# Kernel optimization log

Hardware: AMD Instinct MI355X
Metric: run time of the kernel (lower is better)

The kernel has to match this reference:

```python
import jax, jax.numpy as jnp
import numpy as np

H = 64  # hidden_size


def gru_layer(x, h0, W_ih, W_hh, b_ih, b_hh):
    """PyTorch-convention GRU layer. x: [B,T,D], h0: [B,H]. Returns ([B,T,H], [B,H])."""
    # Precompute input-side gate projections with one big GEMM: [B,T,3H]
    gx_all = jnp.einsum('btd,gd->btg', x, W_ih) + b_ih

    def step(h, gx):
        gh = h @ W_hh.T + b_hh                      # [B,3H]
        xr, xz, xn = jnp.split(gx, 3, axis=-1)
        hr, hz, hn = jnp.split(gh, 3, axis=-1)
        r = jax.nn.sigmoid(xr + hr)
        z = jax.nn.sigmoid(xz + hz)
        n = jnp.tanh(xn + r * hn)
        h_new = (1.0 - z) * n + z * h
        return h_new, h_new

    hT, hs = jax.lax.scan(step, h0, jnp.swapaxes(gx_all, 0, 1))  # hs: [T,B,H]
    return jnp.swapaxes(hs, 0, 1), hT


def setup_inputs() -> dict:
    key = jax.random.key(0)
    ks = jax.random.split(key, 16)
    B, T, D = 256, 2048, 1
    x = jax.random.normal(ks[0], (B, T, D), dtype=jnp.float32)
    h0 = jnp.zeros((2, B, H), dtype=jnp.float32)
    s = 1.0 / np.sqrt(H)
    # Layer 0: input_size=1
    W_ih0 = jax.random.normal(ks[1], (3 * H, D), dtype=jnp.float32) * s
    W_hh0 = jax.random.normal(ks[2], (3 * H, H), dtype=jnp.float32) * s
    b_ih0 = jnp.zeros((3 * H,), dtype=jnp.float32)
    b_hh0 = jnp.zeros((3 * H,), dtype=jnp.float32)
    # Layer 1: input_size=H
    W_ih1 = jax.random.normal(ks[3], (3 * H, H), dtype=jnp.float32) * s
    W_hh1 = jax.random.normal(ks[4], (3 * H, H), dtype=jnp.float32) * s
    b_ih1 = jnp.zeros((3 * H,), dtype=jnp.float32)
    b_hh1 = jnp.zeros((3 * H,), dtype=jnp.float32)
    # Head: Linear(H,H) -> ReLU -> Linear(H,1)
    Wh1 = jax.random.normal(ks[5], (H, H), dtype=jnp.float32) * s
    bh1 = jnp.zeros((H,), dtype=jnp.float32)
    Wh2 = jax.random.normal(ks[6], (1, H), dtype=jnp.float32) * s
    bh2 = jnp.zeros((1,), dtype=jnp.float32)
    return {"x": x, "h0": h0, "W_ih0": W_ih0, "W_hh0": W_hh0, "b_ih0": b_ih0,
            "b_hh0": b_hh0, "W_ih1": W_ih1, "W_hh1": W_hh1, "b_ih1": b_ih1,
            "b_hh1": b_hh1, "Wh1": Wh1, "bh1": bh1, "Wh2": Wh2, "bh2": bh2}


def reference(x, h0, W_ih0, W_hh0, b_ih0, b_hh0, W_ih1, W_hh1, b_ih1, b_hh1,
              Wh1, bh1, Wh2, bh2):
    z0, hT0 = gru_layer(x, h0[0], W_ih0, W_hh0, b_ih0, b_hh0)
    z1, hT1 = gru_layer(z0, h0[1], W_ih1, W_hh1, b_ih1, b_hh1)
    hT = jnp.stack([hT0, hT1], axis=0)           # [2,B,H]
    h = jax.nn.relu(jnp.einsum('bth,oh->bto', z1, Wh1) + bh1)
    y = jnp.einsum('bth,oh->bto', h, Wh2) + bh2  # [B,T,1]
    return (y, hT)
```

## Files before the change

### kernel.cpp

```cpp
#include <hip/hip_runtime.h>

#define HH 64
#define TT 2048
#define BB 256
#define YSZ (BB*TT)

__device__ __forceinline__ float sigmoid_f(float v) {
    return 1.0f / (1.0f + __expf(-v));
}
__device__ __forceinline__ float tanh_f(float v) {
    return 1.0f - 2.0f / (1.0f + __expf(2.0f * v));
}

__global__ __launch_bounds__(512, 2)
void gru_fused(const float* __restrict__ x,
               const float* __restrict__ h0in,
               const float* __restrict__ W_ih0,
               const float* __restrict__ W_hh0,
               const float* __restrict__ b_ih0,
               const float* __restrict__ b_hh0,
               const float* __restrict__ W_ih1,
               const float* __restrict__ W_hh1,
               const float* __restrict__ b_ih1,
               const float* __restrict__ b_hh1,
               const float* __restrict__ Wh1,
               const float* __restrict__ bh1,
               const float* __restrict__ Wh2,
               const float* __restrict__ bh2,
               float* __restrict__ out)
{
    const int b    = blockIdx.x;
    const int tid  = threadIdx.x;
    const int t    = tid & 255;
    const int half = tid >> 8;
    const int ko   = half << 5;

    __shared__ __align__(16) float h0_lds[HH];
    __shared__ __align__(16) float h1_lds[HH];
    __shared__ __align__(16) float part[2 * 192 * 4];
    __shared__ __align__(16) float ph[2 * 64];
    __shared__ __align__(16) float x_lds[TT];

    {
        const float4* xs = reinterpret_cast<const float4*>(x + (size_t)b * TT);
        float4*       xd = reinterpret_cast<float4*>(x_lds);
        for (int k = tid; k < TT / 4; k += 512) xd[k] = xs[k];
    }
    if (tid < HH) {
        h0_lds[tid] = h0in[           b * HH + tid];
        h1_lds[tid] = h0in[BB * HH +  b * HH + tid];
    }

    float4 wA[8], wB[8], wC[8];
    float bA = 0.f, bB = 0.f, bC = 0.f;
    if (t < 192) {
        const float4* pa = reinterpret_cast<const float4*>(W_hh0 + t * HH + ko);
        const float4* pb = reinterpret_cast<const float4*>(W_ih1 + t * HH + ko);
        const float4* pc = reinterpret_cast<const float4*>(W_hh1 + t * HH + ko);
        #pragma unroll
        for (int k = 0; k < 8; ++k) { wA[k] = pa[k]; wB[k] = pb[k]; wC[k] = pc[k]; }
        if (half == 0) { bA = b_hh0[t]; bB = b_ih1[t]; bC = b_hh1[t]; }
    } else {
        const float4* pa = reinterpret_cast<const float4*>(Wh1 + (t - 192) * HH + ko);
        #pragma unroll
        for (int k = 0; k < 8; ++k) { wA[k] = pa[k]; wB[k] = pa[k]; wC[k] = pa[k]; }
    }
    float wih0_r = 0.f, wih0_z = 0.f, wih0_n = 0.f;
    float bih0_r = 0.f, bih0_z = 0.f, bih0_n = 0.f;
    if (tid >= 64 && tid < 128) {
        const int j = tid - 64;
        wih0_r = W_ih0[j];       bih0_r = b_ih0[j];
        wih0_z = W_ih0[j + 64];  bih0_z = b_ih0[j + 64];
        wih0_n = W_ih0[j + 128]; bih0_n = b_ih0[j + 128];
    }
    float wh2_r = 0.f, bhead = 0.f, bh2_s = 0.f;
    if (tid >= 448) {
        const int j = tid - 448;
        wh2_r = Wh2[j]; bhead = bh1[j]; bh2_s = bh2[0];
    }

    __syncthreads();

    const float4* h0q   = reinterpret_cast<const float4*>(h0_lds + ko);
    const float4* h1q   = reinterpret_cast<const float4*>(h1_lds + ko);
    float4*       part4 = reinterpret_cast<float4*>(part);

    for (int i = 0; i <= TT + 1; ++i) {
        if (t < 192) {
            float a0 = bA, a1 = bB, a2 = bC;
            #pragma unroll
            for (int k = 0; k < 8; ++k) {
                float4 u = h0q[k];
                float4 v = h1q[k];
                a0 = fmaf(wA[k].x, u.x, a0); a1 = fmaf(wB[k].x, u.x, a1); a2 = fmaf(wC[k].x, v.x, a2);
                a0 = fmaf(wA[k].y, u.y, a0); a1 = fmaf(wB[k].y, u.y, a1); a2 = fmaf(wC[k].y, v.y, a2);
                a0 = fmaf(wA[k].z, u.z, a0); a1 = fmaf(wB[k].z, u.z, a1); a2 = fmaf(wC[k].z, v.z, a2);
                a0 = fmaf(wA[k].w, u.w, a0); a1 = fmaf(wB[k].w, u.w, a1); a2 = fmaf(wC[k].w, v.w, a2);
            }
            part4[half * 192 + t] = make_float4(a0, a1, a2, 0.f);
        } else {
            float s = 0.f;
            #pragma unroll
            for (int k = 0; k < 8; ++k) {
                float4 v = h1q[k];
                s = fmaf(wA[k].x, v.x, s); s = fmaf(wA[k].y, v.y, s);
                s = fmaf(wA[k].z, v.z, s); s = fmaf(wA[k].w, v.w, s);
            }
            ph[half * 64 + (t - 192)] = s;
        }
        __syncthreads();

        if (tid < 64) {
            const int j = tid;
            float4 q0r = part4[j];       float4 q1r = part4[192 + j];
            float4 q0z = part4[j + 64];  float4 q1z = part4[192 + j + 64];
            float4 q0n = part4[j + 128]; float4 q1n = part4[192 + j + 128];
            float r = sigmoid_f(q0r.y + q1r.y + q0r.z + q1r.z);
            float z = sigmoid_f(q0z.y + q1z.y + q0z.z + q1z.z);
            float n = tanh_f(fmaf(r, q0n.z + q1n.z, q0n.y + q1n.y));
            if (i >= 1 && i <= TT) {
                float hp = h1_lds[j];
                h1_lds[j] = fmaf(z, hp - n, n);
            }
        } else if (tid < 128) {
            const int j  = tid - 64;
            const int xi = (i < TT) ? i : (TT - 1);
            float4 q0r = part4[j];       float4 q1r = part4[192 + j];
            float4 q0z = part4[j + 64];  float4 q1z = part4[192 + j + 64];
            float4 q0n = part4[j + 128]; float4 q1n = part4[192 + j + 128];
            float xv = x_lds[xi];
            float r = sigmoid_f(fmaf(xv, wih0_r, bih0_r) + q0r.x + q1r.x);
            float z = sigmoid_f(fmaf(xv, wih0_z, bih0_z) + q0z.x + q1z.x);
            float n = tanh_f(fmaf(r, q0n.x + q1n.x, fmaf(xv, wih0_n, bih0_n)));
            if (i < TT) {
                float hp = h0_lds[j];
                h0_lds[j] = fmaf(z, hp - n, n);
            }
        } else if (tid >= 448) {
            const int j = tid - 448;
            float s = ph[j] + ph[64 + j] + bhead;
            float p = fmaxf(s, 0.f) * wh2_r;
            #pragma unroll
            for (int m = 1; m < 64; m <<= 1) p += __shfl_xor(p, m, 64);
            if (tid == 448 && i >= 2) out[(size_t)b * TT + (i - 2)] = p + bh2_s;
        }
        __syncthreads();
    }

    if (tid < HH) {
        out[YSZ +           b * HH + tid] = h0_lds[tid];
        out[YSZ + BB * HH + b * HH + tid] = h1_lds[tid];
    }
}

extern "C" void kernel_launch(void* const* d_in, const int* in_sizes, int n_in,
                              void* d_out, int out_size, void* d_ws, size_t ws_size,
                              hipStream_t stream) {
    const float* x     = (const float*)d_in[0];
    const float* h0in  = (const float*)d_in[1];
    const float* W_ih0 = (const float*)d_in[2];
    const float* W_hh0 = (const float*)d_in[3];
    const float* b_ih0 = (const float*)d_in[4];
    const float* b_hh0 = (const float*)d_in[5];
    const float* W_ih1 = (const float*)d_in[6];
    const float* W_hh1 = (const float*)d_in[7];
    const float* b_ih1 = (const float*)d_in[8];
    const float* b_hh1 = (const float*)d_in[9];
    const float* Wh1   = (const float*)d_in[10];
    const float* bh1   = (const float*)d_in[11];
    const float* Wh2   = (const float*)d_in[12];
    const float* bh2   = (const float*)d_in[13];
    float* out = (float*)d_out;

    gru_fused<<<dim3(BB), dim3(512), 0, stream>>>(
        x, h0in, W_ih0, W_hh0, b_ih0, b_hh0,
        W_ih1, W_hh1, b_ih1, b_hh1, Wh1, bh1, Wh2, bh2, out);
}
```

Baseline: 1.702 ms.

## Rewrite GRU recurrence with split-bf16 MFMA matvecs and register-resident state

Replaces the scalar FMA matrix-vector products with v_mfma_f32_16x16x32_bf16. Weights and hidden state are split into hi/lo bf16 pairs (three MFMAs per product) to keep near-fp32 accuracy, and weights and biases are pinned in AGPRs. The block shrinks from 512 to 256 threads, the state is kept in registers and double-buffered in LDS, and each step needs one barrier instead of two. The head output is deferred one more step, and x is read from global memory each step instead of being staged in LDS. This trades extra MFMA work and bf16-split arithmetic for fewer barriers and shorter per-step latency on the serial recurrence.

```diff
diff --git a/kernel.cpp b/kernel.cpp
--- a/kernel.cpp
+++ b/kernel.cpp
@@ -5,14 +5,42 @@
 #define BB 256
 #define YSZ (BB*TT)
 
-__device__ __forceinline__ float sigmoid_f(float v) {
-    return 1.0f / (1.0f + __expf(-v));
-}
-__device__ __forceinline__ float tanh_f(float v) {
-    return 1.0f - 2.0f / (1.0f + __expf(2.0f * v));
-}
-
-__global__ __launch_bounds__(512, 2)
+typedef __attribute__((ext_vector_type(8))) short bf16x8;
+typedef __attribute__((ext_vector_type(4))) float f32x4;
+typedef __attribute__((ext_vector_type(4))) unsigned int u32x4;
+
+__device__ __forceinline__ float sigmoid_f(float v) { return 1.0f/(1.0f+__expf(-v)); }
+__device__ __forceinline__ float tanh_f(float v)    { return 1.0f - 2.0f/(1.0f+__expf(2.0f*v)); }
+
+__device__ __forceinline__ void MFMA(f32x4& d, const bf16x8& a, const bf16x8& b) {
+    asm("v_mfma_f32_16x16x32_bf16 %0, %1, %2, %0" : "+v"(d) : "a"(a), "v"(b));
+}
+#define PIN8(v)  asm("" : "+a"(v))
+#define PINF(v)  asm("" : "+a"(v))
+
+__device__ __forceinline__ void split_pair(float a0, float a1, unsigned& hi, unsigned& lo) {
+    unsigned u0 = __float_as_uint(a0) & 0xFFFF0000u;
+    unsigned u1 = __float_as_uint(a1) & 0xFFFF0000u;
+    hi = (u0 >> 16) | u1;
+    float l0 = a0 - __uint_as_float(u0);
+    float l1 = a1 - __uint_as_float(u1);
+    asm("v_cvt_pk_bf16_f32 %0, %1, %2" : "=v"(lo) : "v"(l0), "v"(l1));
+}
+
+__device__ __forceinline__ void load_frag_pair(const float* Wrow, bf16x8& hi8, bf16x8& lo8) {
+    #pragma unroll
+    for (int jj = 0; jj < 8; ++jj) {
+        float f = Wrow[jj];
+        unsigned uh = __float_as_uint(f) & 0xFFFF0000u;
+        hi8[jj] = (short)(uh >> 16);
+        float lo = f - __uint_as_float(uh);
+        unsigned ul = __float_as_uint(lo);
+        unsigned rr = ul + 0x7FFFu + ((ul >> 16) & 1u);
+        lo8[jj] = (short)(rr >> 16);
+    }
+}
+
+__global__ __launch_bounds__(256, 1)
 void gru_fused(const float* __restrict__ x,
                const float* __restrict__ h0in,
                const float* __restrict__ W_ih0,
@@ -31,125 +59,177 @@
 {
     const int b    = blockIdx.x;
     const int tid  = threadIdx.x;
-    const int t    = tid & 255;
-    const int half = tid >> 8;
-    const int ko   = half << 5;
-
-    __shared__ __align__(16) float h0_lds[HH];
-    __shared__ __align__(16) float h1_lds[HH];
-    __shared__ __align__(16) float part[2 * 192 * 4];
-    __shared__ __align__(16) float ph[2 * 64];
-    __shared__ __align__(16) float x_lds[TT];
-
-    {
-        const float4* xs = reinterpret_cast<const float4*>(x + (size_t)b * TT);
-        float4*       xd = reinterpret_cast<float4*>(x_lds);
-        for (int k = tid; k < TT / 4; k += 512) xd[k] = xs[k];
-    }
-    if (tid < HH) {
-        h0_lds[tid] = h0in[           b * HH + tid];
-        h1_lds[tid] = h0in[BB * HH +  b * HH + tid];
-    }
-
-    float4 wA[8], wB[8], wC[8];
-    float bA = 0.f, bB = 0.f, bC = 0.f;
-    if (t < 192) {
-        const float4* pa = reinterpret_cast<const float4*>(W_hh0 + t * HH + ko);
-        const float4* pb = reinterpret_cast<const float4*>(W_ih1 + t * HH + ko);
-        const float4* pc = reinterpret_cast<const float4*>(W_hh1 + t * HH + ko);
-        #pragma unroll
-        for (int k = 0; k < 8; ++k) { wA[k] = pa[k]; wB[k] = pb[k]; wC[k] = pc[k]; }
-        if (half == 0) { bA = b_hh0[t]; bB = b_ih1[t]; bC = b_hh1[t]; }
-    } else {
-        const float4* pa = reinterpret_cast<const float4*>(Wh1 + (t - 192) * HH + ko);
-        #pragma unroll
-        for (int k = 0; k < 8; ++k) { wA[k] = pa[k]; wB[k] = pa[k]; wC[k] = pa[k]; }
-    }
-    float wih0_r = 0.f, wih0_z = 0.f, wih0_n = 0.f;
-    float bih0_r = 0.f, bih0_z = 0.f, bih0_n = 0.f;
-    if (tid >= 64 && tid < 128) {
-        const int j = tid - 64;
-        wih0_r = W_ih0[j];       bih0_r = b_ih0[j];
-        wih0_z = W_ih0[j + 64];  bih0_z = b_ih0[j + 64];
-        wih0_n = W_ih0[j + 128]; bih0_n = b_ih0[j + 128];
-    }
-    float wh2_r = 0.f, bhead = 0.f, bh2_s = 0.f;
-    if (tid >= 448) {
-        const int j = tid - 448;
-        wh2_r = Wh2[j]; bhead = bh1[j]; bh2_s = bh2[0];
-    }
-
+    const int j    = tid >> 6;
+    const int lane = tid & 63;
+    const int g    = lane >> 4;
+    const int c    = lane & 15;
+
+    __shared__ __align__(16) unsigned int hpk[2][2][2][32];
+    __shared__ float yp[2][4];
+
+    bf16x8 fA[12], fX[12], fG[12], fH[4];
+    #pragma unroll
+    for (int t = 0; t < 3; ++t)
+        #pragma unroll
+        for (int kh = 0; kh < 2; ++kh) {
+            const size_t ro = (size_t)(64*t + 16*j + c) * HH + kh*32 + g*8;
+            load_frag_pair(W_hh0 + ro, fA[t*4+kh*2], fA[t*4+kh*2+1]);
+            load_frag_pair(W_ih1 + ro, fX[t*4+kh*2], fX[t*4+kh*2+1]);
+            load_frag_pair(W_hh1 + ro, fG[t*4+kh*2], fG[t*4+kh*2+1]);
+        }
+    #pragma unroll
+    for (int kh = 0; kh < 2; ++kh)
+        load_frag_pair(Wh1 + (size_t)(16*j + c) * HH + kh*32 + g*8,
+                       fH[kh*2], fH[kh*2+1]);
+    #pragma unroll
+    for (int i = 0; i < 12; ++i) { PIN8(fA[i]); PIN8(fX[i]); PIN8(fG[i]); }
+    #pragma unroll
+    for (int i = 0; i < 4; ++i) PIN8(fH[i]);
+
+    float bA[12], bX[12], bG[12], bH4[4];
+    #pragma unroll
+    for (int t = 0; t < 3; ++t)
+        #pragma unroll
+        for (int r = 0; r < 4; ++r) {
+            const int row = 64*t + 16*j + g*4 + r;
+            bA[t*4+r] = b_hh0[row];
+            bX[t*4+r] = b_ih1[row];
+            bG[t*4+r] = b_hh1[row];
+        }
+    float wR[4], wZ[4], wN[4], bR[4], bZ[4], bN[4], wh2c[4];
+    #pragma unroll
+    for (int r = 0; r < 4; ++r) {
+        const int m = 16*j + g*4 + r;
+        bH4[r]  = bh1[m];
+        wR[r] = W_ih0[m];      bR[r] = b_ih0[m];
+        wZ[r] = W_ih0[m+64];   bZ[r] = b_ih0[m+64];
+        wN[r] = W_ih0[m+128];  bN[r] = b_ih0[m+128];
+        wh2c[r] = Wh2[m];
+    }
+    #pragma unroll
+    for (int i = 0; i < 12; ++i) { PINF(bA[i]); PINF(bX[i]); PINF(bG[i]); }
+    #pragma unroll
+    for (int r = 0; r < 4; ++r) {
+        PINF(bH4[r]); PINF(wR[r]); PINF(wZ[r]); PINF(wN[r]);
+        PINF(bR[r]);  PINF(bZ[r]); PINF(bN[r]); PINF(wh2c[r]);
+    }
+    const float bh2v = bh2[0];
+
+    float h0p[4], h1p[4];
+    #pragma unroll
+    for (int r = 0; r < 4; ++r) {
+        h0p[r] = h0in[          b*HH + 16*j + g*4 + r];
+        h1p[r] = h0in[BB*HH +   b*HH + 16*j + g*4 + r];
+    }
+    if (c == 0) {
+        unsigned ph_, pl_;
+        const int mp = 8*j + g*2;
+        split_pair(h0p[0], h0p[1], ph_, pl_);
+        hpk[0][0][0][mp]   = ph_; hpk[0][0][1][mp]   = pl_;
+        split_pair(h0p[2], h0p[3], ph_, pl_);
+        hpk[0][0][0][mp+1] = ph_; hpk[0][0][1][mp+1] = pl_;
+        split_pair(h1p[0], h1p[1], ph_, pl_);
+        hpk[0][1][0][mp]   = ph_; hpk[0][1][1][mp]   = pl_;
+        split_pair(h1p[2], h1p[3], ph_, pl_);
+        hpk[0][1][0][mp+1] = ph_; hpk[0][1][1][mp+1] = pl_;
+    }
     __syncthreads();
 
-    const float4* h0q   = reinterpret_cast<const float4*>(h0_lds + ko);
-    const float4* h1q   = reinterpret_cast<const float4*>(h1_lds + ko);
-    float4*       part4 = reinterpret_cast<float4*>(part);
-
-    for (int i = 0; i <= TT + 1; ++i) {
-        if (t < 192) {
-            float a0 = bA, a1 = bB, a2 = bC;
+    for (int ii = 0; ii <= TT + 2; ++ii) {
+        const int buf = ii & 1, nbuf = buf ^ 1;
+
+        const float xv = x[(size_t)b*TT + (ii < TT ? ii : TT-1)];
+        if (tid == 0 && ii >= 3) {
+            const int pb = (ii-1) & 1;
+            out[(size_t)b*TT + (ii-3)] =
+                yp[pb][0] + yp[pb][1] + yp[pb][2] + yp[pb][3] + bh2v;
+        }
+        bf16x8 B0h[2], B0l[2], B1h[2], B1l[2];
+        #pragma unroll
+        for (int kh = 0; kh < 2; ++kh) {
+            const int o = kh*16 + g*4;
+            B0h[kh] = __builtin_bit_cast(bf16x8, *(const u32x4*)&hpk[buf][0][0][o]);
+            B0l[kh] = __builtin_bit_cast(bf16x8, *(const u32x4*)&hpk[buf][0][1][o]);
+            B1h[kh] = __builtin_bit_cast(bf16x8, *(const u32x4*)&hpk[buf][1][0][o]);
+            B1l[kh] = __builtin_bit_cast(bf16x8, *(const u32x4*)&hpk[buf][1][1][o]);
+        }
+        f32x4 aA[3], aX[3], aG[3], aH;
+        #pragma unroll
+        for (int t = 0; t < 3; ++t) {
+            aA[t] = (f32x4){bA[t*4+0], bA[t*4+1], bA[t*4+2], bA[t*4+3]};
+            aX[t] = (f32x4){bX[t*4+0], bX[t*4+1], bX[t*4+2], bX[t*4+3]};
+            aG[t] = (f32x4){bG[t*4+0], bG[t*4+1], bG[t*4+2], bG[t*4+3]};
+        }
+        aH = (f32x4){bH4[0], bH4[1], bH4[2], bH4[3]};
+        #pragma unroll
+        for (int t = 0; t < 3; ++t)
             #pragma unroll
-            for (int k = 0; k < 8; ++k) {
-                float4 u = h0q[k];
-                float4 v = h1q[k];
-                a0 = fmaf(wA[k].x, u.x, a0); a1 = fmaf(wB[k].x, u.x, a1); a2 = fmaf(wC[k].x, v.x, a2);
-                a0 = fmaf(wA[k].y, u.y, a0); a1 = fmaf(wB[k].y, u.y, a1); a2 = fmaf(wC[k].y, v.y, a2);
-                a0 = fmaf(wA[k].z, u.z, a0); a1 = fmaf(wB[k].z, u.z, a1); a2 = fmaf(wC[k].z, v.z, a2);
-                a0 = fmaf(wA[k].w, u.w, a0); a1 = fmaf(wB[k].w, u.w, a1); a2 = fmaf(wC[k].w, v.w, a2);
+            for (int kh = 0; kh < 2; ++kh) {
+                const int fi = t*4 + kh*2;
+                MFMA(aA[t], fA[fi],   B0h[kh]);
+                MFMA(aA[t], fA[fi],   B0l[kh]);
+                MFMA(aA[t], fA[fi+1], B0h[kh]);
+                MFMA(aX[t], fX[fi],   B0h[kh]);
+                MFMA(aX[t], fX[fi],   B0l[kh]);
+                MFMA(aX[t], fX[fi+1], B0h[kh]);
+                MFMA(aG[t], fG[fi],   B1h[kh]);
+                MFMA(aG[t], fG[fi],   B1l[kh]);
+                MFMA(aG[t], fG[fi+1], B1h[kh]);
             }
-            part4[half * 192 + t] = make_float4(a0, a1, a2, 0.f);
-        } else {
-            float s = 0.f;
+        #pragma unroll
+        for (int kh = 0; kh < 2; ++kh) {
+            MFMA(aH, fH[kh*2],   B1h[kh]);
+            MFMA(aH, fH[kh*2],   B1l[kh]);
+            MFMA(aH, fH[kh*2+1], B1h[kh]);
+        }
+        {
+            float p = 0.f;
             #pragma unroll
-            for (int k = 0; k < 8; ++k) {
-                float4 v = h1q[k];
-                s = fmaf(wA[k].x, v.x, s); s = fmaf(wA[k].y, v.y, s);
-                s = fmaf(wA[k].z, v.z, s); s = fmaf(wA[k].w, v.w, s);
-            }
-            ph[half * 64 + (t - 192)] = s;
+            for (int r = 0; r < 4; ++r) p = fmaf(fmaxf(aH[r], 0.f), wh2c[r], p);
+            p += __shfl_xor(p, 16, 64);
+            p += __shfl_xor(p, 32, 64);
+            if (lane == 0) yp[ii & 1][j] = p;
+        }
+
+        const bool c1 = (ii >= 1) && (ii <= TT);
+        const bool c0 = (ii < TT);
+        #pragma unroll
+        for (int r = 0; r < 4; ++r) {
+            float rr = sigmoid_f(aX[0][r] + aG[0][r]);
+            float zz = sigmoid_f(aX[1][r] + aG[1][r]);
+            float nn = tanh_f(fmaf(rr, aG[2][r], aX[2][r]));
+            float h1n = fmaf(zz, h1p[r] - nn, nn);
+            h1p[r] = c1 ? h1n : h1p[r];
+            float xr = fmaf(xv, wR[r], bR[r]);
+            float xz = fmaf(xv, wZ[r], bZ[r]);
+            float xn = fmaf(xv, wN[r], bN[r]);
+            float r0 = sigmoid_f(xr + aA[0][r]);
+            float z0 = sigmoid_f(xz + aA[1][r]);
+            float n0 = tanh_f(fmaf(r0, aA[2][r], xn));
+            float h0n = fmaf(z0, h0p[r] - n0, n0);
+            h0p[r] = c0 ? h0n : h0p[r];
+        }
+        if (c == 0) {
+            unsigned ph_, pl_;
+            const int mp = 8*j + g*2;
+            split_pair(h0p[0], h0p[1], ph_, pl_);
+            hpk[nbuf][0][0][mp]   = ph_; hpk[nbuf][0][1][mp]   = pl_;
+            split_pair(h0p[2], h0p[3], ph_, pl_);
+            hpk[nbuf][0][0][mp+1] = ph_; hpk[nbuf][0][1][mp+1] = pl_;
+            split_pair(h1p[0], h1p[1], ph_, pl_);
+            hpk[nbuf][1][0][mp]   = ph_; hpk[nbuf][1][1][mp]   = pl_;
+            split_pair(h1p[2], h1p[3], ph_, pl_);
+            hpk[nbuf][1][0][mp+1] = ph_; hpk[nbuf][1][1][mp+1] = pl_;
         }
         __syncthreads();
-
-        if (tid < 64) {
-            const int j = tid;
-            float4 q0r = part4[j];       float4 q1r = part4[192 + j];
-            float4 q0z = part4[j + 64];  float4 q1z = part4[192 + j + 64];
-            float4 q0n = part4[j + 128]; float4 q1n = part4[192 + j + 128];
-            float r = sigmoid_f(q0r.y + q1r.y + q0r.z + q1r.z);
-            float z = sigmoid_f(q0z.y + q1z.y + q0z.z + q1z.z);
-            float n = tanh_f(fmaf(r, q0n.z + q1n.z, q0n.y + q1n.y));
-            if (i >= 1 && i <= TT) {
-                float hp = h1_lds[j];
-                h1_lds[j] = fmaf(z, hp - n, n);
-            }
-        } else if (tid < 128) {
-            const int j  = tid - 64;
-            const int xi = (i < TT) ? i : (TT - 1);
-            float4 q0r = part4[j];       float4 q1r = part4[192 + j];
-            float4 q0z = part4[j + 64];  float4 q1z = part4[192 + j + 64];
-            float4 q0n = part4[j + 128]; float4 q1n = part4[192 + j + 128];
-            float xv = x_lds[xi];
-            float r = sigmoid_f(fmaf(xv, wih0_r, bih0_r) + q0r.x + q1r.x);
-            float z = sigmoid_f(fmaf(xv, wih0_z, bih0_z) + q0z.x + q1z.x);
-            float n = tanh_f(fmaf(r, q0n.x + q1n.x, fmaf(xv, wih0_n, bih0_n)));
-            if (i < TT) {
-                float hp = h0_lds[j];
-                h0_lds[j] = fmaf(z, hp - n, n);
-            }
-        } else if (tid >= 448) {
-            const int j = tid - 448;
-            float s = ph[j] + ph[64 + j] + bhead;
-            float p = fmaxf(s, 0.f) * wh2_r;
-            #pragma unroll
-            for (int m = 1; m < 64; m <<= 1) p += __shfl_xor(p, m, 64);
-            if (tid == 448 && i >= 2) out[(size_t)b * TT + (i - 2)] = p + bh2_s;
-        }
-        __syncthreads();
-    }
-
-    if (tid < HH) {
-        out[YSZ +           b * HH + tid] = h0_lds[tid];
-        out[YSZ + BB * HH + b * HH + tid] = h1_lds[tid];
+    }
+
+    if (c == 0) {
+        #pragma unroll
+        for (int r = 0; r < 4; ++r) {
+            out[YSZ +           b*HH + 16*j + g*4 + r] = h0p[r];
+            out[YSZ + BB*HH +   b*HH + 16*j + g*4 + r] = h1p[r];
+        }
     }
 }
 
@@ -172,7 +252,7 @@
     const float* bh2   = (const float*)d_in[13];
     float* out = (float*)d_out;
 
-    gru_fused<<<dim3(BB), dim3(512), 0, stream>>>(
+    gru_fused<<<dim3(BB), dim3(256), 0, stream>>>(
         x, h0in, W_ih0, W_hh0, b_ih0, b_hh0,
         W_ih1, W_hh1, b_ih1, b_hh1, Wh1, bh1, Wh2, bh2, out);
 }
```

After: 3.388 ms. +99.1%, slower.
